# Kernel tuning notes

Measured on AMD Instinct MI355X. Metric: run time of the kernel, lower is better.

Reference implementation:

```python
import jax, jax.numpy as jnp
import numpy as np

B, L, D, H = 2, 256, 512, 8
DH = D // H
EPS = 1e-12
NEG = -1000000000000000.0


def setup_inputs() -> dict:
    key = jax.random.key(0)
    ks = jax.random.split(key, 16)
    s = 0.02
    return {
        "inputs": jax.random.normal(ks[0], (B, L, D), jnp.float32),
        "pos_embedding": jax.random.normal(ks[1], (B, L, L, D), jnp.float32),
        "seq_mask": jnp.ones((B, L), jnp.int32),
        "Wq": jax.random.normal(ks[2], (D, D), jnp.float32) * s,
        "bq": jnp.zeros((D,), jnp.float32),
        "Wk": jax.random.normal(ks[3], (D, D), jnp.float32) * s,
        "bk": jnp.zeros((D,), jnp.float32),
        "Wv": jax.random.normal(ks[4], (D, D), jnp.float32) * s,
        "bv": jnp.zeros((D,), jnp.float32),
        "Wr": jax.random.normal(ks[5], (D, D), jnp.float32) * s,
        "br": jnp.zeros((D,), jnp.float32),
        "u": jax.random.normal(ks[6], (H, DH), jnp.float32),
        "v": jax.random.normal(ks[7], (H, DH), jnp.float32),
        "Wf": jax.random.normal(ks[8], (D, D), jnp.float32) * s,
        "bf": jnp.zeros((D,), jnp.float32),
        "gamma": jnp.ones((D,), jnp.float32),
        "beta": jnp.zeros((D,), jnp.float32),
    }


def _layer_norm(x, gamma, beta, eps):
    mu = jnp.mean(x, axis=-1, keepdims=True)
    var = jnp.mean(jnp.square(x - mu), axis=-1, keepdims=True)
    return (x - mu) * jax.lax.rsqrt(var + eps) * gamma + beta


def reference(inputs, pos_embedding, seq_mask, Wq, bq, Wk, bk, Wv, bv, Wr, br,
              u, v, Wf, bf, gamma, beta):
    b, l, d = inputs.shape
    # projections (nn.Linear: x @ W.T + b)
    q = (inputs @ Wq.T + bq).reshape(b, l, H, DH).transpose(0, 2, 1, 3)  # [B,H,L,DH]
    k = (inputs @ Wk.T + bk).reshape(b, l, H, DH).transpose(0, 2, 1, 3)
    vv = (inputs @ Wv.T + bv).reshape(b, l, H, DH).transpose(0, 2, 1, 3)
    rel = (pos_embedding @ Wr.T + br).reshape(b, l, l, H, DH)            # [B,L,L,H,DH]

    # A + C: content-content + content-bias
    A_C = jnp.einsum('bhid,bhjd->bhij', q + u[None, :, None, :], k)
    # B + D: position term against per-(i,j) relative embeddings
    B_D = jnp.einsum('bhid,bijhd->bhij', q + v[None, :, None, :], rel)

    score = (A_C + B_D) / np.sqrt(DH).astype(np.float32)
    invalid = (seq_mask == 0)[:, None, None, :]   # mask keys where seq_mask==0
    score = jnp.where(invalid, NEG, score)
    attn = jax.nn.softmax(score, axis=-1)

    ctx = jnp.einsum('bhij,bhjd->bhid', attn, vv)
    ctx = ctx.transpose(0, 2, 1, 3).reshape(b, l, d)

    # FFN (single dense) + residual + LayerNorm
    h = ctx @ Wf.T + bf
    return _layer_norm(h + inputs, gamma, beta, EPS)
```

## Files before the change

### kernel.cpp

```cpp
#include <hip/hip_runtime.h>
#include <cmath>

typedef __bf16 bf16x8 __attribute__((ext_vector_type(8)));
typedef float f32x4 __attribute__((ext_vector_type(4)));

__device__ __forceinline__ float4 ld4(const float* p) { return *reinterpret_cast<const float4*>(p); }
__device__ __forceinline__ void st4(float* p, float4 v) { *reinterpret_cast<float4*>(p) = v; }
__device__ __forceinline__ void fma4(float4& a, float s, const float4& v) {
    a.x = fmaf(s, v.x, a.x); a.y = fmaf(s, v.y, a.y);
    a.z = fmaf(s, v.z, a.z); a.w = fmaf(s, v.w, a.w);
}
__device__ __forceinline__ float dot4(const float4& a, const float4& b) {
    return a.x*b.x + a.y*b.y + a.z*b.z + a.w*b.w;
}
__device__ __forceinline__ unsigned short f2bf(float f) {
    unsigned int x = __float_as_uint(f);
    unsigned int r = x + 0x7FFFu + ((x >> 16) & 1u);
    return (unsigned short)(r >> 16);
}
__device__ __forceinline__ ushort4 cvt4u(float4 a) {
    ushort4 u;
    u.x = f2bf(a.x); u.y = f2bf(a.y); u.z = f2bf(a.z); u.w = f2bf(a.w);
    return u;
}
__device__ __forceinline__ bf16x8 cvt8(float4 a, float4 b) {
    bf16x8 r;
    r[0] = (__bf16)a.x; r[1] = (__bf16)a.y; r[2] = (__bf16)a.z; r[3] = (__bf16)a.w;
    r[4] = (__bf16)b.x; r[5] = (__bf16)b.y; r[6] = (__bf16)b.z; r[7] = (__bf16)b.w;
    return r;
}

__device__ __forceinline__ void mfma_tile(
        const float* __restrict__ Abase, int ldA,
        const float* __restrict__ Bbase, int ldB,
        int K, int lane, f32x4 acc[4]) {
    int koff = (lane >> 4) * 8;
    int rr = lane & 15;
    const float* ap = Abase + rr * ldA + koff;
    const float* bp = Bbase + rr * ldB + koff;
#pragma unroll 2
    for (int k0 = 0; k0 < K; k0 += 32) {
        float4 a0  = ld4(ap + k0),            a1  = ld4(ap + k0 + 4);
        float4 b00 = ld4(bp + k0),            b01 = ld4(bp + k0 + 4);
        float4 b10 = ld4(bp + 16*ldB + k0),   b11 = ld4(bp + 16*ldB + k0 + 4);
        float4 b20 = ld4(bp + 32*ldB + k0),   b21 = ld4(bp + 32*ldB + k0 + 4);
        float4 b30 = ld4(bp + 48*ldB + k0),   b31 = ld4(bp + 48*ldB + k0 + 4);
        bf16x8 af = cvt8(a0, a1);
        acc[0] = __builtin_amdgcn_mfma_f32_16x16x32_bf16(af, cvt8(b00, b01), acc[0], 0, 0, 0);
        acc[1] = __builtin_amdgcn_mfma_f32_16x16x32_bf16(af, cvt8(b10, b11), acc[1], 0, 0, 0);
        acc[2] = __builtin_amdgcn_mfma_f32_16x16x32_bf16(af, cvt8(b20, b21), acc[2], 0, 0, 0);
        acc[3] = __builtin_amdgcn_mfma_f32_16x16x32_bf16(af, cvt8(b30, b31), acc[3], 0, 0, 0);
    }
}

__global__ __launch_bounds__(256) void k_wrt(
        const float* __restrict__ Wr, float* __restrict__ Wrt) {
    __shared__ float tile[32][33];
    int n0 = blockIdx.x * 32, k0 = blockIdx.y * 32;
    int tx = threadIdx.x & 31, ty = threadIdx.x >> 5;
#pragma unroll
    for (int r = 0; r < 4; r++) {
        int row = ty * 4 + r;
        tile[row][tx] = Wr[(n0 + row) * 512 + k0 + tx];
    }
    __syncthreads();
#pragma unroll
    for (int r = 0; r < 4; r++) {
        int row = ty * 4 + r;
        Wrt[(k0 + row) * 512 + n0 + tx] = tile[tx][row];
    }
}

__global__ __launch_bounds__(256) void k_qkv(
        const float* __restrict__ x,
        const float* __restrict__ Wq, const float* __restrict__ Wk, const float* __restrict__ Wv,
        const float* __restrict__ bq, const float* __restrict__ bk, const float* __restrict__ bv,
        float* __restrict__ qw, float* __restrict__ kw, float* __restrict__ vw) {
    int mat = blockIdx.z;
    const float* W   = (mat == 0) ? Wq : (mat == 1) ? Wk : Wv;
    const float* bias= (mat == 0) ? bq : (mat == 1) ? bk : bv;
    float* out       = (mat == 0) ? qw : (mat == 1) ? kw : vw;
    int m0 = blockIdx.x * 64, n0 = blockIdx.y * 64;
    int t = threadIdx.x, wv = t >> 6, lane = t & 63;
    f32x4 acc[4] = {{0,0,0,0},{0,0,0,0},{0,0,0,0},{0,0,0,0}};
    mfma_tile(x + (m0 + wv * 16) * 512, 512, W + n0 * 512, 512, 512, lane, acc);
    int h = n0 >> 6;
    int col = lane & 15, rbase = (lane >> 4) * 4;
#pragma unroll
    for (int c = 0; c < 4; c++) {
        int d = c * 16 + col;
        float bv_ = bias[n0 + d];
#pragma unroll
        for (int r = 0; r < 4; r++) {
            int m = m0 + wv * 16 + rbase + r;
            int b = m >> 8, i = m & 255;
            out[((b * 8 + h) * 256 + i) * 64 + d] = acc[c][r] + bv_;
        }
    }
}

__global__ __launch_bounds__(256) void k_small(
        const float* __restrict__ qw, const float* __restrict__ kw,
        const float* __restrict__ wrt,
        const float* __restrict__ u, const float* __restrict__ vb,
        const float* __restrict__ br,
        float* __restrict__ c_ws, float* __restrict__ uk_ws, float* __restrict__ vwr_ws) {
    int g = blockIdx.x * 256 + threadIdx.x;
    if (g < 4096) {
        int h = (g >> 8) & 7;
        const float* qrow = qw + g * 64;
        const float* brh = br + h * 64;
        const float* vbh = vb + h * 64;
        float s = 0.f;
#pragma unroll
        for (int d = 0; d < 64; d += 4) {
            float4 q4 = ld4(qrow + d), b4 = ld4(brh + d), v4 = ld4(vbh + d);
            s += (q4.x + v4.x) * b4.x + (q4.y + v4.y) * b4.y
               + (q4.z + v4.z) * b4.z + (q4.w + v4.w) * b4.w;
        }
        c_ws[g] = s;
    } else if (g < 8192) {
        int g2 = g - 4096;
        int h = (g2 >> 8) & 7;
        const float* krow = kw + g2 * 64;
        const float* uh = u + h * 64;
        float s = 0.f;
#pragma unroll
        for (int d = 0; d < 64; d += 4) s += dot4(ld4(krow + d), ld4(uh + d));
        uk_ws[g2] = s;
    } else if (g < 12288) {
        int g3 = g - 8192;
        int h = g3 >> 9, e = g3 & 511;
        const float* wr_row = wrt + e * 512 + h * 64;
        const float* vbh = vb + h * 64;
        float s = 0.f;
#pragma unroll
        for (int d = 0; d < 64; d += 4) s += dot4(ld4(wr_row + d), ld4(vbh + d));
        vwr_ws[h * 512 + e] = s;
    }
}

__global__ __launch_bounds__(256) void k_w(
        const float* __restrict__ qw, const float* __restrict__ wrt,
        const float* __restrict__ vwr_ws, float* __restrict__ w_ws) {
    int h = blockIdx.z;
    int m0 = blockIdx.x * 64, n0 = blockIdx.y * 64;
    int t = threadIdx.x, wv = t >> 6, lane = t & 63;
    int b = m0 >> 8, i0 = m0 & 255;
    f32x4 acc[4] = {{0,0,0,0},{0,0,0,0},{0,0,0,0},{0,0,0,0}};
    mfma_tile(qw + ((b * 8 + h) * 256 + i0 + wv * 16) * 64, 64,
              wrt + n0 * 512 + h * 64, 512, 64, lane, acc);
    int col = lane & 15, rbase = (lane >> 4) * 4;
#pragma unroll
    for (int c = 0; c < 4; c++) {
        int n = n0 + c * 16 + col;
        float vw_ = vwr_ws[h * 512 + n];
#pragma unroll
        for (int r = 0; r < 4; r++) {
            int m = m0 + wv * 16 + rbase + r;
            w_ws[((size_t)m * 8 + h) * 512 + n] = acc[c][r] + vw_;
        }
    }
}

__global__ __launch_bounds__(256) void k_ac(
        const float* __restrict__ qw, const float* __restrict__ kw,
        const float* __restrict__ uk_ws, const float* __restrict__ c_ws,
        float* __restrict__ ac_ws) {
    int bh = blockIdx.z;
    int b = bh >> 3, h = bh & 7;
    int i0 = blockIdx.x * 64, j0 = blockIdx.y * 64;
    int t = threadIdx.x, wv = t >> 6, lane = t & 63;
    f32x4 acc[4] = {{0,0,0,0},{0,0,0,0},{0,0,0,0},{0,0,0,0}};
    mfma_tile(qw + ((b * 8 + h) * 256 + i0 + wv * 16) * 64, 64,
              kw + ((b * 8 + h) * 256 + j0) * 64, 64, 64, lane, acc);
    int col = lane & 15, rbase = (lane >> 4) * 4;
#pragma unroll
    for (int c = 0; c < 4; c++) {
        int j = j0 + c * 16 + col;
        float ukv = uk_ws[(b * 8 + h) * 256 + j];
#pragma unroll
        for (int r = 0; r < 4; r++) {
            int i = i0 + wv * 16 + rbase + r;
            ac_ws[((b * 256 + i) * 8 + h) * 256 + j] = acc[c][r] + ukv + c_ws[(b * 8 + h) * 256 + i];
        }
    }
}

__global__ __launch_bounds__(512, 4) void k_attn(
        const float* __restrict__ pos, const float* __restrict__ w_ws,
        const float* __restrict__ ac_ws, const float* __restrict__ vw,
        const int* __restrict__ seq_mask, float* __restrict__ ctx) {
    int bi = blockIdx.x;
    int b = bi >> 8, i = bi & 255;
    int t = threadIdx.x;
    int wv = t >> 6, lane = t & 63;
    __shared__ unsigned short wl[8 * 512];
    __shared__ float sc[8][256];
    __shared__ unsigned short stage[8][4096];

    {
        int h = t >> 6;
        int e0 = (t & 63) * 8;
        const float* src = w_ws + ((size_t)bi * 8 + h) * 512 + e0;
        float4 a = ld4(src);
        float4 c = ld4(src + 4);
        *reinterpret_cast<ushort4*>(&wl[h * 512 + e0])     = cvt4u(a);
        *reinterpret_cast<ushort4*>(&wl[h * 512 + e0 + 4]) = cvt4u(c);
    }
    __syncthreads();

    const float* pb = pos + (size_t)bi * (256 * 512);
    int jbase = wv * 32;
    unsigned short* sb = &stage[wv][0];
    int arow = lane & 15;
    int koff = (lane >> 4) * 8;

#pragma unroll
    for (int jt = 0; jt < 2; jt++) {
        f32x4 acc = {0, 0, 0, 0};
#pragma unroll
        for (int eh = 0; eh < 2; eh++) {
            const float* src = pb + (size_t)(jbase + jt * 16) * 512 + eh * 256 + lane * 4;
            float4 tmp[16];
#pragma unroll
            for (int s = 0; s < 16; s++) tmp[s] = ld4(src + s * 512);
#pragma unroll
            for (int s = 0; s < 16; s++) {
                *reinterpret_cast<ushort4*>(&sb[s * 256 + lane * 4]) = cvt4u(tmp[s]);
            }
#pragma unroll
            for (int es = 0; es < 8; es++) {
                bf16x8 af = *reinterpret_cast<const bf16x8*>(&sb[arow * 256 + es * 32 + koff]);
                bf16x8 bf = *reinterpret_cast<const bf16x8*>(&wl[(lane & 7) * 512 + (eh * 8 + es) * 32 + koff]);
                acc = __builtin_amdgcn_mfma_f32_16x16x32_bf16(af, bf, acc, 0, 0, 0);
            }
        }
        int h = lane & 15;
        int rbase = (lane >> 4) * 4;
        if (h < 8) {
#pragma unroll
            for (int r = 0; r < 4; r++) sc[h][jbase + jt * 16 + rbase + r] = acc[r];
        }
    }
    __syncthreads();

    {
        int h = wv;
        const float* acrow = ac_ws + ((b * 256 + i) * 8 + h) * 256;
        float vals[4];
        float mx = -INFINITY;
#pragma unroll
        for (int r = 0; r < 4; r++) {
            int j = lane + r * 64;
            float s = (sc[h][j] + acrow[j]) * 0.125f;
            if (seq_mask[b * 256 + j] == 0) s = -1e15f;
            vals[r] = s;
            mx = fmaxf(mx, s);
        }
#pragma unroll
        for (int m = 32; m >= 1; m >>= 1) mx = fmaxf(mx, __shfl_xor(mx, m, 64));
        float sum = 0.f;
#pragma unroll
        for (int r = 0; r < 4; r++) { vals[r] = __expf(vals[r] - mx); sum += vals[r]; }
#pragma unroll
        for (int m = 32; m >= 1; m >>= 1) sum += __shfl_xor(sum, m, 64);
        float inv = 1.0f / sum;
#pragma unroll
        for (int r = 0; r < 4; r++) sc[h][lane + r * 64] = vals[r] * inv;
    }

    float4* part = reinterpret_cast<float4*>(&stage[0][0]);
    {
        int h = wv;
        int d4 = (lane & 15) * 4;
        int js = lane >> 4;
        const float* vbase = vw + (size_t)(b * 8 + h) * 256 * 64;
        float4 acc = {0, 0, 0, 0};
        for (int r = 0; r < 64; r++) {
            int j = js * 64 + r;
            float p = sc[h][j];
            float4 v4 = ld4(&vbase[j * 64 + d4]);
            fma4(acc, p, v4);
        }
        part[(h * 4 + js) * 16 + (lane & 15)] = acc;
    }
    {
        int h = wv;
        if ((lane >> 4) == 0) {
            int l = lane & 15;
            float4 a0 = part[(h * 4 + 0) * 16 + l], a1 = part[(h * 4 + 1) * 16 + l];
            float4 a2 = part[(h * 4 + 2) * 16 + l], a3 = part[(h * 4 + 3) * 16 + l];
            float4 o;
            o.x = a0.x + a1.x + a2.x + a3.x;
            o.y = a0.y + a1.y + a2.y + a3.y;
            o.z = a0.z + a1.z + a2.z + a3.z;
            o.w = a0.w + a1.w + a2.w + a3.w;
            st4(ctx + (size_t)(b * 256 + i) * 512 + h * 64 + l * 4, o);
        }
    }
}

__global__ __launch_bounds__(256) void k_ffn(
        const float* __restrict__ A, const float* __restrict__ Wf,
        const float* __restrict__ bias, const float* __restrict__ resid,
        float* __restrict__ outp) {
    int m0 = blockIdx.x * 64, n0 = blockIdx.y * 64;
    int t = threadIdx.x, wv = t >> 6, lane = t & 63;
    f32x4 acc[4] = {{0,0,0,0},{0,0,0,0},{0,0,0,0},{0,0,0,0}};
    mfma_tile(A + (m0 + wv * 16) * 512, 512, Wf + n0 * 512, 512, 512, lane, acc);
    int col = lane & 15, rbase = (lane >> 4) * 4;
#pragma unroll
    for (int c = 0; c < 4; c++) {
        int n = n0 + c * 16 + col;
        float bv_ = bias[n];
#pragma unroll
        for (int r = 0; r < 4; r++) {
            int m = m0 + wv * 16 + rbase + r;
            outp[m * 512 + n] = acc[c][r] + bv_ + resid[m * 512 + n];
        }
    }
}

__global__ __launch_bounds__(256) void k_ln(
        const float* __restrict__ tmp, const float* __restrict__ gamma,
        const float* __restrict__ beta, float* __restrict__ out) {
    int m = blockIdx.x, t = threadIdx.x;
    int wv = t >> 6, lane = t & 63;
    float2 xv = *reinterpret_cast<const float2*>(&tmp[m * 512 + t * 2]);
    __shared__ float red[4];
    float s = xv.x + xv.y;
#pragma unroll
    for (int k = 32; k >= 1; k >>= 1) s += __shfl_xor(s, k, 64);
    if (lane == 0) red[wv] = s;
    __syncthreads();
    float mu = (red[0] + red[1] + red[2] + red[3]) * (1.0f / 512.0f);
    __syncthreads();
    float dx = xv.x - mu, dy = xv.y - mu;
    float vs = dx * dx + dy * dy;
#pragma unroll
    for (int k = 32; k >= 1; k >>= 1) vs += __shfl_xor(vs, k, 64);
    if (lane == 0) red[wv] = vs;
    __syncthreads();
    float var = (red[0] + red[1] + red[2] + red[3]) * (1.0f / 512.0f);
    float rstd = rsqrtf(var + 1e-12f);
    float2 g = *reinterpret_cast<const float2*>(&gamma[t * 2]);
    float2 be = *reinterpret_cast<const float2*>(&beta[t * 2]);
    float2 o;
    o.x = dx * rstd * g.x + be.x;
    o.y = dy * rstd * g.y + be.y;
    *reinterpret_cast<float2*>(&out[m * 512 + t * 2]) = o;
}

extern "C" void kernel_launch(void* const* d_in, const int* in_sizes, int n_in,
                              void* d_out, int out_size, void* d_ws, size_t ws_size,
                              hipStream_t stream) {
    const float* x     = (const float*)d_in[0];
    const float* pos   = (const float*)d_in[1];
    const int*   smask = (const int*)d_in[2];
    const float* Wq = (const float*)d_in[3];
    const float* bq = (const float*)d_in[4];
    const float* Wk = (const float*)d_in[5];
    const float* bk = (const float*)d_in[6];
    const float* Wv = (const float*)d_in[7];
    const float* bv = (const float*)d_in[8];
    const float* Wr = (const float*)d_in[9];
    const float* br = (const float*)d_in[10];
    const float* u  = (const float*)d_in[11];
    const float* vb = (const float*)d_in[12];
    const float* Wf = (const float*)d_in[13];
    const float* bf = (const float*)d_in[14];
    const float* gamma = (const float*)d_in[15];
    const float* beta  = (const float*)d_in[16];
    float* out = (float*)d_out;

    float* ws = (float*)d_ws;
    float* q_ws   = ws;
    float* k_ws   = q_ws  + 262144;
    float* v_ws   = k_ws  + 262144;
    float* w_ws   = v_ws  + 262144;
    float* c_ws   = w_ws  + 2097152;
    float* uk_ws  = c_ws  + 4096;
    float* vwr_ws = uk_ws + 4096;
    float* ac_ws  = vwr_ws + 4096;
    float* ctx_ws = ac_ws + 1048576;
    float* tmp_ws = ctx_ws + 262144;
    float* wrt_ws = tmp_ws + 262144;

    k_wrt<<<dim3(16, 16), 256, 0, stream>>>(Wr, wrt_ws);
    k_qkv<<<dim3(8, 8, 3), 256, 0, stream>>>(x, Wq, Wk, Wv, bq, bk, bv, q_ws, k_ws, v_ws);
    k_small<<<dim3(48), 256, 0, stream>>>(q_ws, k_ws, wrt_ws, u, vb, br, c_ws, uk_ws, vwr_ws);
    k_w<<<dim3(8, 8, 8), 256, 0, stream>>>(q_ws, wrt_ws, vwr_ws, w_ws);
    k_ac<<<dim3(4, 4, 16), 256, 0, stream>>>(q_ws, k_ws, uk_ws, c_ws, ac_ws);
    k_attn<<<dim3(512), 512, 0, stream>>>(pos, w_ws, ac_ws, v_ws, smask, ctx_ws);
    k_ffn<<<dim3(8, 8), 256, 0, stream>>>(ctx_ws, Wf, bf, x, tmp_ws);
    k_ln<<<dim3(512), 256, 0, stream>>>(tmp_ws, gamma, beta, out);
}
```

Measured before the change: 117.3 us.

## Merge front-end kernels into two launches and unroll PV accumulation

Merges the Wr transpose and QKV projection into one launch, and merges the small bias-dot kernel with the W and AC GEMMs. Each block now computes the bias dot products it needs (vwr, c, uk) into shared memory instead of reading them from a separate pass. This cuts the launch count from five to two and removes a tiny serial kernel. The cost is some redundant dot-product work per block. The attention PV loop is also unrolled by four to issue more independent loads per iteration.

```diff
diff --git a/kernel.cpp b/kernel.cpp
--- a/kernel.cpp
+++ b/kernel.cpp
@@ -53,136 +53,138 @@
     }
 }
 
-__global__ __launch_bounds__(256) void k_wrt(
-        const float* __restrict__ Wr, float* __restrict__ Wrt) {
-    __shared__ float tile[32][33];
-    int n0 = blockIdx.x * 32, k0 = blockIdx.y * 32;
-    int tx = threadIdx.x & 31, ty = threadIdx.x >> 5;
-#pragma unroll
-    for (int r = 0; r < 4; r++) {
-        int row = ty * 4 + r;
-        tile[row][tx] = Wr[(n0 + row) * 512 + k0 + tx];
-    }
-    __syncthreads();
-#pragma unroll
-    for (int r = 0; r < 4; r++) {
-        int row = ty * 4 + r;
-        Wrt[(k0 + row) * 512 + n0 + tx] = tile[tx][row];
-    }
-}
-
-__global__ __launch_bounds__(256) void k_qkv(
+__global__ __launch_bounds__(256) void k_front(
         const float* __restrict__ x,
         const float* __restrict__ Wq, const float* __restrict__ Wk, const float* __restrict__ Wv,
         const float* __restrict__ bq, const float* __restrict__ bk, const float* __restrict__ bv,
-        float* __restrict__ qw, float* __restrict__ kw, float* __restrict__ vw) {
-    int mat = blockIdx.z;
-    const float* W   = (mat == 0) ? Wq : (mat == 1) ? Wk : Wv;
-    const float* bias= (mat == 0) ? bq : (mat == 1) ? bk : bv;
-    float* out       = (mat == 0) ? qw : (mat == 1) ? kw : vw;
-    int m0 = blockIdx.x * 64, n0 = blockIdx.y * 64;
-    int t = threadIdx.x, wv = t >> 6, lane = t & 63;
-    f32x4 acc[4] = {{0,0,0,0},{0,0,0,0},{0,0,0,0},{0,0,0,0}};
-    mfma_tile(x + (m0 + wv * 16) * 512, 512, W + n0 * 512, 512, 512, lane, acc);
-    int h = n0 >> 6;
-    int col = lane & 15, rbase = (lane >> 4) * 4;
-#pragma unroll
-    for (int c = 0; c < 4; c++) {
-        int d = c * 16 + col;
-        float bv_ = bias[n0 + d];
-#pragma unroll
-        for (int r = 0; r < 4; r++) {
-            int m = m0 + wv * 16 + rbase + r;
-            int b = m >> 8, i = m & 255;
-            out[((b * 8 + h) * 256 + i) * 64 + d] = acc[c][r] + bv_;
-        }
-    }
-}
-
-__global__ __launch_bounds__(256) void k_small(
+        const float* __restrict__ Wr,
+        float* __restrict__ qw, float* __restrict__ kw, float* __restrict__ vw,
+        float* __restrict__ wrt) {
+    int id = blockIdx.x;
+    int t = threadIdx.x;
+    if (id < 192) {
+        int mat = id >> 6, rem = id & 63;
+        int m0 = (rem >> 3) * 64, n0 = (rem & 7) * 64;
+        const float* W   = (mat == 0) ? Wq : (mat == 1) ? Wk : Wv;
+        const float* bias= (mat == 0) ? bq : (mat == 1) ? bk : bv;
+        float* out       = (mat == 0) ? qw : (mat == 1) ? kw : vw;
+        int wv = t >> 6, lane = t & 63;
+        f32x4 acc[4] = {{0,0,0,0},{0,0,0,0},{0,0,0,0},{0,0,0,0}};
+        mfma_tile(x + (m0 + wv * 16) * 512, 512, W + n0 * 512, 512, 512, lane, acc);
+        int h = n0 >> 6;
+        int col = lane & 15, rbase = (lane >> 4) * 4;
+#pragma unroll
+        for (int c = 0; c < 4; c++) {
+            int d = c * 16 + col;
+            float bv_ = bias[n0 + d];
+#pragma unroll
+            for (int r = 0; r < 4; r++) {
+                int m = m0 + wv * 16 + rbase + r;
+                int b = m >> 8, i = m & 255;
+                out[((b * 8 + h) * 256 + i) * 64 + d] = acc[c][r] + bv_;
+            }
+        }
+    } else {
+        __shared__ float tile[64][65];
+        int id2 = id - 192;
+        int n0 = (id2 >> 3) * 64, k0 = (id2 & 7) * 64;
+        int tx = t & 63, ty = t >> 6;
+#pragma unroll
+        for (int r = 0; r < 16; r++) {
+            int row = ty * 16 + r;
+            tile[row][tx] = Wr[(n0 + row) * 512 + k0 + tx];
+        }
+        __syncthreads();
+#pragma unroll
+        for (int r = 0; r < 16; r++) {
+            int row = ty * 16 + r;
+            wrt[(k0 + row) * 512 + n0 + tx] = tile[tx][row];
+        }
+    }
+}
+
+__global__ __launch_bounds__(256) void k_mid(
         const float* __restrict__ qw, const float* __restrict__ kw,
         const float* __restrict__ wrt,
-        const float* __restrict__ u, const float* __restrict__ vb,
-        const float* __restrict__ br,
-        float* __restrict__ c_ws, float* __restrict__ uk_ws, float* __restrict__ vwr_ws) {
-    int g = blockIdx.x * 256 + threadIdx.x;
-    if (g < 4096) {
-        int h = (g >> 8) & 7;
-        const float* qrow = qw + g * 64;
-        const float* brh = br + h * 64;
-        const float* vbh = vb + h * 64;
-        float s = 0.f;
-#pragma unroll
-        for (int d = 0; d < 64; d += 4) {
-            float4 q4 = ld4(qrow + d), b4 = ld4(brh + d), v4 = ld4(vbh + d);
-            s += (q4.x + v4.x) * b4.x + (q4.y + v4.y) * b4.y
-               + (q4.z + v4.z) * b4.z + (q4.w + v4.w) * b4.w;
-        }
-        c_ws[g] = s;
-    } else if (g < 8192) {
-        int g2 = g - 4096;
-        int h = (g2 >> 8) & 7;
-        const float* krow = kw + g2 * 64;
-        const float* uh = u + h * 64;
-        float s = 0.f;
-#pragma unroll
-        for (int d = 0; d < 64; d += 4) s += dot4(ld4(krow + d), ld4(uh + d));
-        uk_ws[g2] = s;
-    } else if (g < 12288) {
-        int g3 = g - 8192;
-        int h = g3 >> 9, e = g3 & 511;
-        const float* wr_row = wrt + e * 512 + h * 64;
-        const float* vbh = vb + h * 64;
-        float s = 0.f;
-#pragma unroll
-        for (int d = 0; d < 64; d += 4) s += dot4(ld4(wr_row + d), ld4(vbh + d));
-        vwr_ws[h * 512 + e] = s;
-    }
-}
-
-__global__ __launch_bounds__(256) void k_w(
-        const float* __restrict__ qw, const float* __restrict__ wrt,
-        const float* __restrict__ vwr_ws, float* __restrict__ w_ws) {
-    int h = blockIdx.z;
-    int m0 = blockIdx.x * 64, n0 = blockIdx.y * 64;
+        const float* __restrict__ u, const float* __restrict__ vb, const float* __restrict__ br,
+        float* __restrict__ w_ws, float* __restrict__ ac_ws) {
+    int id = blockIdx.x;
     int t = threadIdx.x, wv = t >> 6, lane = t & 63;
-    int b = m0 >> 8, i0 = m0 & 255;
-    f32x4 acc[4] = {{0,0,0,0},{0,0,0,0},{0,0,0,0},{0,0,0,0}};
-    mfma_tile(qw + ((b * 8 + h) * 256 + i0 + wv * 16) * 64, 64,
-              wrt + n0 * 512 + h * 64, 512, 64, lane, acc);
-    int col = lane & 15, rbase = (lane >> 4) * 4;
-#pragma unroll
-    for (int c = 0; c < 4; c++) {
-        int n = n0 + c * 16 + col;
-        float vw_ = vwr_ws[h * 512 + n];
-#pragma unroll
-        for (int r = 0; r < 4; r++) {
-            int m = m0 + wv * 16 + rbase + r;
-            w_ws[((size_t)m * 8 + h) * 512 + n] = acc[c][r] + vw_;
-        }
-    }
-}
-
-__global__ __launch_bounds__(256) void k_ac(
-        const float* __restrict__ qw, const float* __restrict__ kw,
-        const float* __restrict__ uk_ws, const float* __restrict__ c_ws,
-        float* __restrict__ ac_ws) {
-    int bh = blockIdx.z;
-    int b = bh >> 3, h = bh & 7;
-    int i0 = blockIdx.x * 64, j0 = blockIdx.y * 64;
-    int t = threadIdx.x, wv = t >> 6, lane = t & 63;
-    f32x4 acc[4] = {{0,0,0,0},{0,0,0,0},{0,0,0,0},{0,0,0,0}};
-    mfma_tile(qw + ((b * 8 + h) * 256 + i0 + wv * 16) * 64, 64,
-              kw + ((b * 8 + h) * 256 + j0) * 64, 64, 64, lane, acc);
-    int col = lane & 15, rbase = (lane >> 4) * 4;
-#pragma unroll
-    for (int c = 0; c < 4; c++) {
-        int j = j0 + c * 16 + col;
-        float ukv = uk_ws[(b * 8 + h) * 256 + j];
-#pragma unroll
-        for (int r = 0; r < 4; r++) {
-            int i = i0 + wv * 16 + rbase + r;
-            ac_ws[((b * 256 + i) * 8 + h) * 256 + j] = acc[c][r] + ukv + c_ws[(b * 8 + h) * 256 + i];
+    __shared__ float red[8][64];
+    if (id < 512) {
+        int h = id >> 6, rem = id & 63;
+        int m0 = (rem >> 3) * 64, n0 = (rem & 7) * 64;
+        int b = m0 >> 8, i0 = m0 & 255;
+        {
+            int e = t & 63, grp = t >> 6;
+            const float* wr_row = wrt + (size_t)(n0 + e) * 512 + h * 64 + grp * 16;
+            const float* vbh = vb + h * 64 + grp * 16;
+            float s = 0.f;
+#pragma unroll
+            for (int d = 0; d < 16; d += 4) s += dot4(ld4(wr_row + d), ld4(vbh + d));
+            red[grp][e] = s;
+        }
+        __syncthreads();
+        __shared__ float vwr_l[64];
+        if (t < 64) vwr_l[t] = red[0][t] + red[1][t] + red[2][t] + red[3][t];
+        f32x4 acc[4] = {{0,0,0,0},{0,0,0,0},{0,0,0,0},{0,0,0,0}};
+        mfma_tile(qw + ((b * 8 + h) * 256 + i0 + wv * 16) * 64, 64,
+                  wrt + (size_t)n0 * 512 + h * 64, 512, 64, lane, acc);
+        __syncthreads();
+        int col = lane & 15, rbase = (lane >> 4) * 4;
+#pragma unroll
+        for (int c = 0; c < 4; c++) {
+            float vw_ = vwr_l[c * 16 + col];
+            int n = n0 + c * 16 + col;
+#pragma unroll
+            for (int r = 0; r < 4; r++) {
+                int m = m0 + wv * 16 + rbase + r;
+                w_ws[((size_t)m * 8 + h) * 512 + n] = acc[c][r] + vw_;
+            }
+        }
+    } else {
+        int id2 = id - 512;
+        int bh = id2 >> 4, rem2 = id2 & 15;
+        int b = bh >> 3, h = bh & 7;
+        int i0 = (rem2 >> 2) * 64, j0 = (rem2 & 3) * 64;
+        {
+            int xx = t & 63, grp = t >> 6;
+            const float* qrow = qw + ((b * 8 + h) * 256 + i0 + xx) * 64 + grp * 16;
+            const float* brh = br + h * 64 + grp * 16;
+            const float* vbh = vb + h * 64 + grp * 16;
+            float s = 0.f;
+#pragma unroll
+            for (int d = 0; d < 16; d += 4) {
+                float4 q4 = ld4(qrow + d), b4 = ld4(brh + d), v4 = ld4(vbh + d);
+                s += (q4.x + v4.x) * b4.x + (q4.y + v4.y) * b4.y
+                   + (q4.z + v4.z) * b4.z + (q4.w + v4.w) * b4.w;
+            }
+            red[grp][xx] = s;
+            const float* krow = kw + ((b * 8 + h) * 256 + j0 + xx) * 64 + grp * 16;
+            const float* uh = u + h * 64 + grp * 16;
+            s = 0.f;
+#pragma unroll
+            for (int d = 0; d < 16; d += 4) s += dot4(ld4(krow + d), ld4(uh + d));
+            red[4 + grp][xx] = s;
+        }
+        __syncthreads();
+        __shared__ float c_l[64], uk_l[64];
+        if (t < 64) c_l[t] = red[0][t] + red[1][t] + red[2][t] + red[3][t];
+        else if (t < 128) { int y = t - 64; uk_l[y] = red[4][y] + red[5][y] + red[6][y] + red[7][y]; }
+        f32x4 acc[4] = {{0,0,0,0},{0,0,0,0},{0,0,0,0},{0,0,0,0}};
+        mfma_tile(qw + ((b * 8 + h) * 256 + i0 + wv * 16) * 64, 64,
+                  kw + ((b * 8 + h) * 256 + j0) * 64, 64, 64, lane, acc);
+        __syncthreads();
+        int col = lane & 15, rbase = (lane >> 4) * 4;
+#pragma unroll
+        for (int c = 0; c < 4; c++) {
+            int j = j0 + c * 16 + col;
+            float ukv = uk_l[c * 16 + col];
+#pragma unroll
+            for (int r = 0; r < 4; r++) {
+                int ii = wv * 16 + rbase + r;
+                ac_ws[((b * 256 + i0 + ii) * 8 + h) * 256 + j] = acc[c][r] + ukv + c_l[ii];
+            }
         }
     }
 }
@@ -275,13 +277,19 @@
         int h = wv;
         int d4 = (lane & 15) * 4;
         int js = lane >> 4;
-        const float* vbase = vw + (size_t)(b * 8 + h) * 256 * 64;
+        const float* vbase = vw + (size_t)(b * 8 + h) * 256 * 64 + d4;
         float4 acc = {0, 0, 0, 0};
-        for (int r = 0; r < 64; r++) {
+#pragma unroll 2
+        for (int r = 0; r < 64; r += 4) {
             int j = js * 64 + r;
-            float p = sc[h][j];
-            float4 v4 = ld4(&vbase[j * 64 + d4]);
-            fma4(acc, p, v4);
+            float p0 = sc[h][j + 0], p1 = sc[h][j + 1];
+            float p2 = sc[h][j + 2], p3 = sc[h][j + 3];
+            float4 v0 = ld4(vbase + (size_t)(j + 0) * 64);
+            float4 v1 = ld4(vbase + (size_t)(j + 1) * 64);
+            float4 v2 = ld4(vbase + (size_t)(j + 2) * 64);
+            float4 v3 = ld4(vbase + (size_t)(j + 3) * 64);
+            fma4(acc, p0, v0); fma4(acc, p1, v1);
+            fma4(acc, p2, v2); fma4(acc, p3, v3);
         }
         part[(h * 4 + js) * 16 + (lane & 15)] = acc;
     }
@@ -379,19 +387,14 @@
     float* k_ws   = q_ws  + 262144;
     float* v_ws   = k_ws  + 262144;
     float* w_ws   = v_ws  + 262144;
-    float* c_ws   = w_ws  + 2097152;
-    float* uk_ws  = c_ws  + 4096;
-    float* vwr_ws = uk_ws + 4096;
-    float* ac_ws  = vwr_ws + 4096;
+    float* ac_ws  = w_ws  + 2097152;
     float* ctx_ws = ac_ws + 1048576;
     float* tmp_ws = ctx_ws + 262144;
     float* wrt_ws = tmp_ws + 262144;
 
-    k_wrt<<<dim3(16, 16), 256, 0, stream>>>(Wr, wrt_ws);
-    k_qkv<<<dim3(8, 8, 3), 256, 0, stream>>>(x, Wq, Wk, Wv, bq, bk, bv, q_ws, k_ws, v_ws);
-    k_small<<<dim3(48), 256, 0, stream>>>(q_ws, k_ws, wrt_ws, u, vb, br, c_ws, uk_ws, vwr_ws);
-    k_w<<<dim3(8, 8, 8), 256, 0, stream>>>(q_ws, wrt_ws, vwr_ws, w_ws);
-    k_ac<<<dim3(4, 4, 16), 256, 0, stream>>>(q_ws, k_ws, uk_ws, c_ws, ac_ws);
+    k_front<<<dim3(256), 256, 0, stream>>>(x, Wq, Wk, Wv, bq, bk, bv, Wr,
+                                           q_ws, k_ws, v_ws, wrt_ws);
+    k_mid<<<dim3(768), 256, 0, stream>>>(q_ws, k_ws, wrt_ws, u, vb, br, w_ws, ac_ws);
     k_attn<<<dim3(512), 512, 0, stream>>>(pos, w_ws, ac_ws, v_ws, smask, ctx_ws);
     k_ffn<<<dim3(8, 8), 256, 0, stream>>>(ctx_ws, Wf, bf, x, tmp_ws);
     k_ln<<<dim3(512), 256, 0, stream>>>(tmp_ws, gamma, beta, out);
```

New measurement: 110.7 us. -5.7%, faster.
